# Optimization experiments

Hardware: AMD Instinct MI355X
Metric: run time of the kernel (lower is better)

Reference implementation:

```python
import jax, jax.numpy as jnp
import numpy as np

H = 256  # hidden size

def _lstm_layer(x, W_ih, W_hh, b_ih, b_hh):
    """x: [B, T, I] -> outputs [B, T, H]. PyTorch gate order: i, f, g, o."""
    B, T, _ = x.shape
    # Precompute input projections for all timesteps at once: [B, T, 4H]
    xg = jnp.einsum('bti,gi->btg', x, W_ih) + (b_ih + b_hh)
    xg = jnp.transpose(xg, (1, 0, 2))  # [T, B, 4H]

    def step(carry, xg_t):
        h, c = carry
        gates = xg_t + h @ W_hh.T  # [B, 4H]
        i = jax.nn.sigmoid(gates[:, 0 * H:1 * H])
        f = jax.nn.sigmoid(gates[:, 1 * H:2 * H])
        g = jnp.tanh(gates[:, 2 * H:3 * H])
        o = jax.nn.sigmoid(gates[:, 3 * H:4 * H])
        c = f * c + i * g
        h = o * jnp.tanh(c)
        return (h, c), h

    h0 = jnp.zeros((B, H), dtype=x.dtype)
    c0 = jnp.zeros((B, H), dtype=x.dtype)
    _, ys = jax.lax.scan(step, (h0, c0), xg)  # ys: [T, B, H]
    return jnp.transpose(ys, (1, 0, 2))


def setup_inputs() -> dict:
    key = jax.random.key(0)
    ks = jax.random.split(key, 9)
    B, T, I = 256, 512, 32
    s_in = 1.0 / np.sqrt(H)
    return {
        'M': jax.random.normal(ks[0], (B, T, I), dtype=jnp.float32),
        'W_ih0': jax.random.normal(ks[1], (4 * H, I), dtype=jnp.float32) * s_in,
        'W_hh0': jax.random.normal(ks[2], (4 * H, H), dtype=jnp.float32) * s_in,
        'b_ih0': jax.random.normal(ks[3], (4 * H,), dtype=jnp.float32) * s_in,
        'b_hh0': jax.random.normal(ks[4], (4 * H,), dtype=jnp.float32) * s_in,
        'W_ih1': jax.random.normal(ks[5], (4 * H, H), dtype=jnp.float32) * s_in,
        'W_hh1': jax.random.normal(ks[6], (4 * H, H), dtype=jnp.float32) * s_in,
        'b_ih1': jax.random.normal(ks[7], (4 * H,), dtype=jnp.float32) * s_in,
        'b_hh1': jax.random.normal(ks[8], (4 * H,), dtype=jnp.float32) * s_in,
    }


def reference(M, W_ih0, W_hh0, b_ih0, b_hh0, W_ih1, W_hh1, b_ih1, b_hh1):
    # observations_preprocessor = Identity
    x = _lstm_layer(M, W_ih0, W_hh0, b_ih0, b_hh0)
    x = _lstm_layer(x, W_ih1, W_hh1, b_ih1, b_hh1)
    # hn = rnn_out[:, -1, :]
    return x[:, -1, :]
```

## Files before the change

### kernel.cpp

```cpp
#include <hip/hip_runtime.h>
#include <hip/hip_fp16.h>


#define TT 512
#define HH 256
#define GS 294912

typedef _Float16 f16x8 __attribute__((ext_vector_type(8)));
typedef float    f32x4 __attribute__((ext_vector_type(4)));
typedef unsigned u32x4 __attribute__((ext_vector_type(4)));

__device__ __forceinline__ f16x8 cvt8(const float* p) {
  const float4 a = *(const float4*)p;
  const float4 b = *(const float4*)(p + 4);
  f16x8 r;
  r[0]=(_Float16)a.x; r[1]=(_Float16)a.y; r[2]=(_Float16)a.z; r[3]=(_Float16)a.w;
  r[4]=(_Float16)b.x; r[5]=(_Float16)b.y; r[6]=(_Float16)b.z; r[7]=(_Float16)b.w;
  return r;
}
__device__ __forceinline__ float sigm(float x){ return 1.f/(1.f + __expf(-x)); }
__device__ __forceinline__ float tanh_(float x){ return 1.f - 2.f/(1.f + __expf(2.f*x)); }

__device__ __forceinline__ u32x4 ld16(const void* p) {
  u32x4 r;
  asm volatile("global_load_dwordx4 %0, %1, off sc0 sc1"
               : "=v"(r) : "v"(p) : "memory");
  return r;
}
__device__ __forceinline__ void st2(void* p, unsigned v) {
  asm volatile("global_store_short %0, %1, off sc0 sc1"
               :: "v"(p), "v"(v) : "memory");
}
__device__ __forceinline__ void stp(void* p, unsigned v) {
  asm volatile("global_store_dword %0, %1, off sc0 sc1"
               :: "v"(p), "v"(v) : "memory");
}
__device__ __forceinline__ unsigned ldp(const void* p) {
  unsigned r;
  asm volatile("global_load_dword %0, %1, off sc0 sc1\n\ts_waitcnt vmcnt(0)"
               : "=v"(r) : "v"(p) : "memory");
  return r;
}
__device__ __forceinline__ u32x4 ldp4(const void* p) {
  u32x4 r;
  asm volatile("global_load_dwordx4 %0, %1, off sc0 sc1\n\ts_waitcnt vmcnt(0)"
               : "=v"(r) : "v"(p) : "memory");
  return r;
}
__device__ __forceinline__ void wvm0() {
  asm volatile("s_waitcnt vmcnt(0)" ::: "memory");
  __builtin_amdgcn_sched_barrier(0);
}
__device__ __forceinline__ void barrier_lds() {
  __builtin_amdgcn_sched_barrier(0);
  asm volatile("s_waitcnt lgkmcnt(0)" ::: "memory");
  __builtin_amdgcn_s_barrier();
  __builtin_amdgcn_sched_barrier(0);
}

__global__ void init_ws(uint4* p, int n) {
  int i = blockIdx.x * blockDim.x + threadIdx.x;
  if (i >= n) return;
  int rem = i % (GS / 16);
  p[i] = (rem < 17408) ? make_uint4(0x00010001u,0x00010001u,0x00010001u,0x00010001u)
                       : make_uint4(0u,0u,0u,0u);
}

__global__ __launch_bounds__(256, 1) void lstm_v16(
    const float* __restrict__ M,
    const float* __restrict__ Wih0, const float* __restrict__ Whh0,
    const float* __restrict__ bih0, const float* __restrict__ bhh0,
    const float* __restrict__ Wih1, const float* __restrict__ Whh1,
    const float* __restrict__ bih1, const float* __restrict__ bhh1,
    float* __restrict__ out, char* __restrict__ ws)
{
  __shared__ __align__(16) char ldsA[16384];
  __shared__ __align__(16) char ldsB[16384];

  const int tid  = threadIdx.x, lane = tid & 63, wv = tid >> 6;
  const int bid  = blockIdx.x;
  const int g    = bid / 12;
  const int idx  = bid - g * 12;
  const int role = idx >> 2;
  const int q4   = idx & 3;
  const int col16 = lane & 15, ko8 = (lane >> 4) << 3, brow = (lane >> 4) << 2;
  const int unit = q4 * 64 + wv * 16 + col16;

  char* base   = ws + (size_t)g * GS;
  char* stream = base;
  char* h1r    = base + 131072;
  char* xg     = base + 147456;
  int*  prog   = (int*)(base + 278528);

  const unsigned ubase = ((unsigned)(unit >> 5) << 10)
                       | ((unsigned)((unit >> 3) & 3) << 8)
                       | ((unsigned)(unit & 7) << 1);

  f16x8 W[4][8], WI[4];
  float bias[4] = {0.f, 0.f, 0.f, 0.f};
  {
    const float* Wsrc = (role == 0) ? Whh0 : (role == 1) ? Wih1 : Whh1;
    #pragma unroll
    for (int q = 0; q < 4; ++q) {
      const int row = q * HH + unit;
      #pragma unroll
      for (int kt = 0; kt < 8; ++kt)
        W[q][kt] = cvt8(Wsrc + (size_t)row * HH + kt * 32 + ko8);
      if (role == 0) { WI[q] = cvt8(Wih0 + (size_t)row * 32 + ko8);
                       bias[q] = bih0[row] + bhh0[row]; }
      else if (role == 1) bias[q] = bih1[row] + bhh1[row];
    }
  }

  float cst[4] = {0.f, 0.f, 0.f, 0.f};

  if (role == 0) {
    const float* mp = M + (size_t)(g * 16 + col16) * TT * 32 + ko8;
    float4 m0 = *(const float4*)mp, m1 = *(const float4*)(mp + 4);
    int lastW = 0;
    for (int t = 0; t < TT; ++t) {
      const int par = t & 1;
      if (t >= 1) {
        const char* s = stream + (size_t)((t - 1) & 15) * 8192 + tid * 16;
        const unsigned pat = (((unsigned)(t - 1) >> 4) & 1u) * 0x00010001u;
        u32x4 v0 = ld16(s), v1 = ld16(s + 4096);
        wvm0();
        for (;;) {
          const u32x4 d = ((v0 ^ pat) | (v1 ^ pat)) & 0x00010001u;
          if (__all((d[0] | d[1] | d[2] | d[3]) == 0)) break;
          v0 = ld16(s); v1 = ld16(s + 4096);
          wvm0();
        }
        *(u32x4*)(ldsA + par * 8192 + tid * 16)        = v0;
        *(u32x4*)(ldsA + par * 8192 + tid * 16 + 4096) = v1;
      }
      barrier_lds();
      f32x4 acc[4];
      f16x8 am;
      am[0]=(_Float16)m0.x; am[1]=(_Float16)m0.y; am[2]=(_Float16)m0.z; am[3]=(_Float16)m0.w;
      am[4]=(_Float16)m1.x; am[5]=(_Float16)m1.y; am[6]=(_Float16)m1.z; am[7]=(_Float16)m1.w;
      #pragma unroll
      for (int q = 0; q < 4; ++q) {
        acc[q] = (f32x4){bias[q], bias[q], bias[q], bias[q]};
        acc[q] = __builtin_amdgcn_mfma_f32_16x16x32_f16(am, WI[q], acc[q], 0, 0, 0);
      }
      if (t >= 1) {
        #pragma unroll
        for (int kt = 0; kt < 8; ++kt) {
          const f16x8 A = *(const f16x8*)(ldsA + par * 8192 + kt * 1024 + lane * 16);
          #pragma unroll
          for (int q = 0; q < 4; ++q)
            acc[q] = __builtin_amdgcn_mfma_f32_16x16x32_f16(A, W[q][kt], acc[q], 0, 0, 0);
        }
      }
      if (t + 1 < TT) { m0 = *(const float4*)(mp + (t + 1) * 32);
                        m1 = *(const float4*)(mp + (t + 1) * 32 + 4); }
      if (t >= 16) {
        while (lastW < t - 15) {
          const u32x4 d = ldp4(prog);
          int m = (int)d[0];
          m = m < (int)d[1] ? m : (int)d[1];
          m = m < (int)d[2] ? m : (int)d[2];
          m = m < (int)d[3] ? m : (int)d[3];
          lastW = m;
        }
      }
      char* slot = stream + (size_t)(t & 15) * 8192;
      const unsigned wt = ((unsigned)t >> 4) & 1u;
      #pragma unroll
      for (int r = 0; r < 4; ++r) {
        const float iv = sigm(acc[0][r]), fv = sigm(acc[1][r]);
        const float gv = tanh_(acc[2][r]), ov = sigm(acc[3][r]);
        cst[r] = fv * cst[r] + iv * gv;
        const float h = ov * tanh_(cst[r]);
        unsigned short hb = __builtin_bit_cast(unsigned short, (_Float16)h);
        hb = (unsigned short)((hb & 0xFFFEu) | wt);
        st2(slot + ubase + ((unsigned)(brow + r) << 4), (unsigned)hb);
      }
    }
  } else if (role == 1) {
    int lastL = 0;
    for (int t = 0; t < TT; ++t) {
      const int par = t & 1;
      {
        const char* s = stream + (size_t)(t & 15) * 8192 + tid * 16;
        const unsigned pat = (((unsigned)t >> 4) & 1u) * 0x00010001u;
        u32x4 v0 = ld16(s), v1 = ld16(s + 4096);
        wvm0();
        for (;;) {
          const u32x4 d = ((v0 ^ pat) | (v1 ^ pat)) & 0x00010001u;
          if (__all((d[0] | d[1] | d[2] | d[3]) == 0)) break;
          v0 = ld16(s); v1 = ld16(s + 4096);
          wvm0();
        }
        *(u32x4*)(ldsA + par * 8192 + tid * 16)        = v0;
        *(u32x4*)(ldsA + par * 8192 + tid * 16 + 4096) = v1;
      }
      barrier_lds();
      if (tid == 0) stp(prog + q4, (unsigned)(t + 1));
      if (t >= 4) { while (lastL < t - 3) lastL = (int)ldp(prog + 4 + q4); }
      f32x4 acc[4];
      #pragma unroll
      for (int q = 0; q < 4; ++q)
        acc[q] = (f32x4){bias[q], bias[q], bias[q], bias[q]};
      #pragma unroll
      for (int kt = 0; kt < 8; ++kt) {
        const f16x8 A = *(const f16x8*)(ldsA + par * 8192 + kt * 1024 + lane * 16);
        #pragma unroll
        for (int q = 0; q < 4; ++q)
          acc[q] = __builtin_amdgcn_mfma_f32_16x16x32_f16(A, W[q][kt], acc[q], 0, 0, 0);
      }
      char* xs = xg + (size_t)(t & 3) * 32768 + q4 * 8192;
      const unsigned wtx = ((unsigned)t >> 2) & 1u;
      #pragma unroll
      for (int q = 0; q < 4; ++q)
        #pragma unroll
        for (int r = 0; r < 4; ++r) {
          unsigned short hb = __builtin_bit_cast(unsigned short, (_Float16)acc[q][r]);
          hb = (unsigned short)((hb & 0xFFFEu) | wtx);
          const unsigned off = (unsigned)(brow + r) * 512
                             + (unsigned)(q * 64 + wv * 16 + col16) * 2;
          st2(xs + off, (unsigned)hb);
        }
    }
  } else {
    for (int t = 0; t < TT; ++t) {
      const int par = t & 1;
      {
        const char* sx = xg + (size_t)(t & 3) * 32768 + q4 * 8192 + tid * 16;
        const unsigned patX = (((unsigned)t >> 2) & 1u) * 0x00010001u;
        const char* sh = h1r + (size_t)((t - 1) & 1) * 8192 + tid * 16;
        const unsigned patH = (((unsigned)(t - 1) >> 1) & 1u) * 0x00010001u;
        const bool hasH = (t >= 1);
        u32x4 x0 = ld16(sx), x1 = ld16(sx + 4096), h0v, h1v;
        if (hasH) { h0v = ld16(sh); h1v = ld16(sh + 4096); }
        wvm0();
        for (;;) {
          u32x4 d = ((x0 ^ patX) | (x1 ^ patX)) & 0x00010001u;
          unsigned bad = d[0] | d[1] | d[2] | d[3];
          if (hasH) {
            const u32x4 e = ((h0v ^ patH) | (h1v ^ patH)) & 0x00010001u;
            bad |= e[0] | e[1] | e[2] | e[3];
          }
          if (__all(bad == 0)) break;
          x0 = ld16(sx); x1 = ld16(sx + 4096);
          if (hasH) { h0v = ld16(sh); h1v = ld16(sh + 4096); }
          wvm0();
        }
        *(u32x4*)(ldsB + par * 8192 + tid * 16)        = x0;
        *(u32x4*)(ldsB + par * 8192 + tid * 16 + 4096) = x1;
        if (hasH) {
          *(u32x4*)(ldsA + par * 8192 + tid * 16)        = h0v;
          *(u32x4*)(ldsA + par * 8192 + tid * 16 + 4096) = h1v;
        }
      }
      barrier_lds();
      if (tid == 0) stp(prog + 4 + q4, (unsigned)(t + 1));
      f32x4 acc[4];
      #pragma unroll
      for (int q = 0; q < 4; ++q) acc[q] = (f32x4){0.f, 0.f, 0.f, 0.f};
      if (t >= 1) {
        #pragma unroll
        for (int kt = 0; kt < 8; ++kt) {
          const f16x8 A = *(const f16x8*)(ldsA + par * 8192 + kt * 1024 + lane * 16);
          #pragma unroll
          for (int q = 0; q < 4; ++q)
            acc[q] = __builtin_amdgcn_mfma_f32_16x16x32_f16(A, W[q][kt], acc[q], 0, 0, 0);
        }
      }
      const char* xl = ldsB + par * 8192;
      #pragma unroll
      for (int q = 0; q < 4; ++q)
        #pragma unroll
        for (int r = 0; r < 4; ++r) {
          const unsigned short xv = *(const unsigned short*)
            (xl + (brow + r) * 512 + (q * 64 + wv * 16 + col16) * 2);
          acc[q][r] += (float)__builtin_bit_cast(_Float16, xv);
        }
      char* d1 = h1r + (size_t)par * 8192;
      const unsigned wt = ((unsigned)t >> 1) & 1u;
      #pragma unroll
      for (int r = 0; r < 4; ++r) {
        const float iv = sigm(acc[0][r]), fv = sigm(acc[1][r]);
        const float gv = tanh_(acc[2][r]), ov = sigm(acc[3][r]);
        cst[r] = fv * cst[r] + iv * gv;
        const float h = ov * tanh_(cst[r]);
        if (t < TT - 1) {
          unsigned short hb = __builtin_bit_cast(unsigned short, (_Float16)h);
          hb = (unsigned short)((hb & 0xFFFEu) | wt);
          st2(d1 + ubase + ((unsigned)(brow + r) << 4), (unsigned)hb);
        } else {
          out[(size_t)(g * 16 + brow + r) * HH + unit] = h;
        }
      }
    }
  }
}

__global__ void fb_init(uint4* p, int n) {
  int i = blockIdx.x * blockDim.x + threadIdx.x;
  if (i < n) p[i] = make_uint4(0x00010001u,0x00010001u,0x00010001u,0x00010001u);
}
__device__ __forceinline__ unsigned fb_tg(int t){ return ((unsigned)(t + 4) >> 1) & 1u; }

__global__ __launch_bounds__(512) void lstm_v9(
    const float* __restrict__ M,
    const float* __restrict__ Wih0, const float* __restrict__ Whh0,
    const float* __restrict__ bih0, const float* __restrict__ bhh0,
    const float* __restrict__ Wih1, const float* __restrict__ Whh1,
    const float* __restrict__ bih1, const float* __restrict__ bhh1,
    float* __restrict__ out, char* __restrict__ ws)
{
  __shared__ __align__(16) char  ldsA[16384];
  __shared__ __align__(16) f32x4 xch[8][64];
  const int tid  = threadIdx.x, lane = tid & 63, wv = tid >> 6;
  const int g = blockIdx.x & 7, w = blockIdx.x >> 3;
  const int hf = wv & 1, role = wv >> 1;
  const int col16 = lane & 15, ko8 = (lane >> 4) << 3;
  const int unit = w * 16 + col16;
  #define H0R(slot) (ws + (((g << 1) | (slot)) << 14))
  #define H1R(slot) (ws + 262144 + (((g << 1) | (slot)) << 14))
  f16x8 W0[4][8], WI[4];
  float bias[4] = {0.f, 0.f, 0.f, 0.f};
  if (role == 0) {
    #pragma unroll
    for (int q = 0; q < 4; ++q) {
      const int row = q * HH + unit;
      #pragma unroll
      for (int kt = 0; kt < 8; ++kt) W0[q][kt] = cvt8(Whh0 + (size_t)row*HH + kt*32 + ko8);
      WI[q] = cvt8(Wih0 + (size_t)row*32 + ko8); bias[q] = bih0[row] + bhh0[row];
    }
  } else if (role == 1) {
    #pragma unroll
    for (int q = 0; q < 4; ++q) {
      const int row = q * HH + unit;
      #pragma unroll
      for (int kt = 0; kt < 8; ++kt) W0[q][kt] = cvt8(Wih1 + (size_t)row*HH + kt*32 + ko8);
      bias[q] = bih1[row] + bhh1[row];
    }
  } else if (role == 2) {
    #pragma unroll
    for (int q = 0; q < 4; ++q) {
      const int row = q * HH + unit;
      #pragma unroll
      for (int kt = 0; kt < 8; ++kt) W0[q][kt] = cvt8(Whh1 + (size_t)row*HH + kt*32 + ko8);
    }
  }
  const int sl = tid & 63, skt = (tid >> 6) & 7;
  const unsigned moff0 = (unsigned)((sl & 15) * 512 + skt * 64 + (sl >> 4) * 16);
  const unsigned moff1 = moff0 + 16 * 512;
  const unsigned lo    = (unsigned)(skt * 1024 + sl * 16);
  const unsigned hoff = (((unsigned)(hf*16 + col16)) << 9) | ((unsigned)(lane >> 4) << 4);
  unsigned soff[4];
  #pragma unroll
  for (int r = 0; r < 4; ++r)
    soff[r] = (((unsigned)(hf*16 + ((lane>>4)<<2) + r)) << 9) | ((unsigned)unit << 1);
  const float* mp = M + (size_t)(g*32 + hf*16 + col16) * TT * 32 + ko8;
  float4 m0 = {0,0,0,0}, m1 = {0,0,0,0};
  if (role == 0) { m0 = *(const float4*)mp; m1 = *(const float4*)(mp + 4); }
  float cst[4] = {0.f, 0.f, 0.f, 0.f};
  for (int p = 0; p <= TT; ++p) {
    if (p >= 1) {
      const char* s = H0R((p - 1) & 1);
      const unsigned pat = fb_tg(p - 1) * 0x00010001u;
      u32x4 v0 = ld16(s + moff0), v1 = ld16(s + moff1);
      wvm0();
      for (;;) {
        const u32x4 d = ((v0 ^ pat) | (v1 ^ pat)) & 0x00010001u;
        if (__all((d[0] | d[1] | d[2] | d[3]) == 0)) break;
        v0 = ld16(s + moff0); v1 = ld16(s + moff1); wvm0();
      }
      *(u32x4*)(ldsA + lo) = v0; *(u32x4*)(ldsA + 8192 + lo) = v1;
    }
    barrier_lds();
    f32x4 acc[4];
    if (role == 0 && p < TT) {
      f16x8 am;
      am[0]=(_Float16)m0.x; am[1]=(_Float16)m0.y; am[2]=(_Float16)m0.z; am[3]=(_Float16)m0.w;
      am[4]=(_Float16)m1.x; am[5]=(_Float16)m1.y; am[6]=(_Float16)m1.z; am[7]=(_Float16)m1.w;
      #pragma unroll
      for (int q = 0; q < 4; ++q) {
        acc[q] = (f32x4){bias[q], bias[q], bias[q], bias[q]};
        acc[q] = __builtin_amdgcn_mfma_f32_16x16x32_f16(am, WI[q], acc[q], 0, 0, 0);
      }
      if (p >= 1) {
        #pragma unroll
        for (int kt = 0; kt < 8; ++kt) {
          const f16x8 A = *(const f16x8*)(ldsA + hf*8192 + kt*1024 + lane*16);
          #pragma unroll
          for (int q = 0; q < 4; ++q)
            acc[q] = __builtin_amdgcn_mfma_f32_16x16x32_f16(A, W0[q][kt], acc[q], 0, 0, 0);
        }
      }
      char* d = H0R(p & 1);
      const unsigned wt = fb_tg(p);
      #pragma unroll
      for (int r = 0; r < 4; ++r) {
        const float iv = sigm(acc[0][r]), fv = sigm(acc[1][r]);
        const float gv = tanh_(acc[2][r]), ov = sigm(acc[3][r]);
        cst[r] = fv * cst[r] + iv * gv;
        const float h = ov * tanh_(cst[r]);
        unsigned short hb = __builtin_bit_cast(unsigned short, (_Float16)h);
        hb = (unsigned short)((hb & 0xFFFEu) | wt);
        st2(d + soff[r], (unsigned)hb);
      }
      if (p + 1 < TT) { m0 = *(const float4*)(mp + (p+1)*32); m1 = *(const float4*)(mp + (p+1)*32 + 4); }
    } else if (role == 1 && p >= 1) {
      #pragma unroll
      for (int q = 0; q < 4; ++q) acc[q] = (f32x4){bias[q], bias[q], bias[q], bias[q]};
      #pragma unroll
      for (int kt = 0; kt < 8; ++kt) {
        const f16x8 A = *(const f16x8*)(ldsA + hf*8192 + kt*1024 + lane*16);
        #pragma unroll
        for (int q = 0; q < 4; ++q)
          acc[q] = __builtin_amdgcn_mfma_f32_16x16x32_f16(A, W0[q][kt], acc[q], 0, 0, 0);
      }
    } else if (role == 2 && p >= 2) {
      const char* s = H1R(p & 1);
      const unsigned pat = fb_tg(p - 2) * 0x00010001u;
      u32x4 hb[8];
      #pragma unroll
      for (int k = 0; k < 8; ++k) hb[k] = ld16(s + hoff + k*64);
      wvm0();
      for (;;) {
        unsigned bad = 0;
        #pragma unroll
        for (int k = 0; k < 8; ++k) {
          const u32x4 d = (hb[k] ^ pat) & 0x00010001u;
          bad |= d[0] | d[1] | d[2] | d[3];
        }
        if (__all(bad == 0)) break;
        #pragma unroll
        for (int k = 0; k < 8; ++k) hb[k] = ld16(s + hoff + k*64);
        wvm0();
      }
      #pragma unroll
      for (int q = 0; q < 4; ++q) acc[q] = (f32x4){0.f, 0.f, 0.f, 0.f};
      #pragma unroll
      for (int kt = 0; kt < 8; ++kt) {
        const f16x8 A = __builtin_bit_cast(f16x8, hb[kt]);
        #pragma unroll
        for (int q = 0; q < 4; ++q)
          acc[q] = __builtin_amdgcn_mfma_f32_16x16x32_f16(A, W0[q][kt], acc[q], 0, 0, 0);
      }
      #pragma unroll
      for (int q = 0; q < 4; ++q) xch[hf*4 + q][lane] = acc[q];
    }
    barrier_lds();
    if (role == 1 && p >= 1) {
      if (p >= 2) {
        #pragma unroll
        for (int q = 0; q < 4; ++q) acc[q] = acc[q] + xch[hf*4 + q][lane];
      }
      if (p < TT) {
        char* d = H1R((p - 1) & 1);
        const unsigned wt = fb_tg(p - 1);
        #pragma unroll
        for (int r = 0; r < 4; ++r) {
          const float iv = sigm(acc[0][r]), fv = sigm(acc[1][r]);
          const float gv = tanh_(acc[2][r]), ov = sigm(acc[3][r]);
          cst[r] = fv * cst[r] + iv * gv;
          const float h = ov * tanh_(cst[r]);
          unsigned short hb = __builtin_bit_cast(unsigned short, (_Float16)h);
          hb = (unsigned short)((hb & 0xFFFEu) | wt);
          st2(d + soff[r], (unsigned)hb);
        }
      } else {
        #pragma unroll
        for (int r = 0; r < 4; ++r) {
          const float iv = sigm(acc[0][r]), fv = sigm(acc[1][r]);
          const float gv = tanh_(acc[2][r]), ov = sigm(acc[3][r]);
          cst[r] = fv * cst[r] + iv * gv;
          const float h = ov * tanh_(cst[r]);
          const int b = hf*16 + ((lane>>4)<<2) + r;
          out[(size_t)(g*32 + b) * HH + (w*16 + col16)] = h;
        }
      }
    }
  }
  #undef H0R
  #undef H1R
}

extern "C" void kernel_launch(void* const* d_in, const int* in_sizes, int n_in,
                              void* d_out, int out_size, void* d_ws, size_t ws_size,
                              hipStream_t stream) {
  (void)in_sizes; (void)n_in; (void)out_size;
  const float* M    = (const float*)d_in[0];
  const float* Wih0 = (const float*)d_in[1];
  const float* Whh0 = (const float*)d_in[2];
  const float* bih0 = (const float*)d_in[3];
  const float* bhh0 = (const float*)d_in[4];
  const float* Wih1 = (const float*)d_in[5];
  const float* Whh1 = (const float*)d_in[6];
  const float* bih1 = (const float*)d_in[7];
  const float* bhh1 = (const float*)d_in[8];

  if (ws_size >= (size_t)16 * GS) {
    const int n16 = 16 * (GS / 16);
    init_ws<<<(n16 + 255) / 256, 256, 0, stream>>>((uint4*)d_ws, n16);
    lstm_v16<<<192, 256, 0, stream>>>(M, Wih0, Whh0, bih0, bhh0,
                                      Wih1, Whh1, bih1, bhh1,
                                      (float*)d_out, (char*)d_ws);
  } else {
    if (ws_size < 524288) return;
    fb_init<<<128, 256, 0, stream>>>((uint4*)d_ws, 32768);
    lstm_v9<<<128, 512, 0, stream>>>(M, Wih0, Whh0, bih0, bhh0,
                                     Wih1, Whh1, bih1, bhh1,
                                     (float*)d_out, (char*)d_ws);
  }
}
```

Before: 1.199 ms.

## Fuse layer-1 input projection into layer-0 blocks, dropping a role

The separate role that computed the layer-1 input projection (W_ih1·h0) is merged into the layer-0 blocks. Each layer-0 block now holds both W_hh0 and W_ih1 in registers and projects h0 of the previous step right after its own recurrence step. The grid shrinks from 12 to 8 blocks per batch group, and the layer-0 back-pressure polling on the projection role's progress counters goes away. The next stream load is also issued early, before the barrier. In exchange, register pressure doubles in the layer-0 role and the projection work now sits on the layer-0 critical path.

```diff
diff --git a/kernel.cpp b/kernel.cpp
--- a/kernel.cpp
+++ b/kernel.cpp
@@ -41,12 +41,6 @@
                : "=v"(r) : "v"(p) : "memory");
   return r;
 }
-__device__ __forceinline__ u32x4 ldp4(const void* p) {
-  u32x4 r;
-  asm volatile("global_load_dwordx4 %0, %1, off sc0 sc1\n\ts_waitcnt vmcnt(0)"
-               : "=v"(r) : "v"(p) : "memory");
-  return r;
-}
 __device__ __forceinline__ void wvm0() {
   asm volatile("s_waitcnt vmcnt(0)" ::: "memory");
   __builtin_amdgcn_sched_barrier(0);
@@ -66,7 +60,7 @@
                        : make_uint4(0u,0u,0u,0u);
 }
 
-__global__ __launch_bounds__(256, 1) void lstm_v16(
+__global__ __launch_bounds__(256, 1) void lstm_v17(
     const float* __restrict__ M,
     const float* __restrict__ Wih0, const float* __restrict__ Whh0,
     const float* __restrict__ bih0, const float* __restrict__ bhh0,
@@ -79,8 +73,8 @@
 
   const int tid  = threadIdx.x, lane = tid & 63, wv = tid >> 6;
   const int bid  = blockIdx.x;
-  const int g    = bid / 12;
-  const int idx  = bid - g * 12;
+  const int g    = bid >> 3;
+  const int idx  = bid & 7;
   const int role = idx >> 2;
   const int q4   = idx & 3;
   const int col16 = lane & 15, ko8 = (lane >> 4) << 3, brow = (lane >> 4) << 2;
@@ -96,19 +90,28 @@
                        | ((unsigned)((unit >> 3) & 3) << 8)
                        | ((unsigned)(unit & 7) << 1);
 
-  f16x8 W[4][8], WI[4];
-  float bias[4] = {0.f, 0.f, 0.f, 0.f};
-  {
-    const float* Wsrc = (role == 0) ? Whh0 : (role == 1) ? Wih1 : Whh1;
+  f16x8 W0[4][8], W1q[4][8], WI[4];
+  float bias0[4] = {0,0,0,0}, bias1[4] = {0,0,0,0};
+  if (role == 0) {
     #pragma unroll
     for (int q = 0; q < 4; ++q) {
       const int row = q * HH + unit;
       #pragma unroll
+      for (int kt = 0; kt < 8; ++kt) {
+        W0[q][kt]  = cvt8(Whh0 + (size_t)row * HH + kt * 32 + ko8);
+        W1q[q][kt] = cvt8(Wih1 + (size_t)row * HH + kt * 32 + ko8);
+      }
+      WI[q]    = cvt8(Wih0 + (size_t)row * 32 + ko8);
+      bias0[q] = bih0[row] + bhh0[row];
+      bias1[q] = bih1[row] + bhh1[row];
+    }
+  } else {
+    #pragma unroll
+    for (int q = 0; q < 4; ++q) {
+      const int row = q * HH + unit;
+      #pragma unroll
       for (int kt = 0; kt < 8; ++kt)
-        W[q][kt] = cvt8(Wsrc + (size_t)row * HH + kt * 32 + ko8);
-      if (role == 0) { WI[q] = cvt8(Wih0 + (size_t)row * 32 + ko8);
-                       bias[q] = bih0[row] + bhh0[row]; }
-      else if (role == 1) bias[q] = bih1[row] + bhh1[row];
+        W0[q][kt] = cvt8(Whh1 + (size_t)row * HH + kt * 32 + ko8);
     }
   }
 
@@ -117,13 +120,13 @@
   if (role == 0) {
     const float* mp = M + (size_t)(g * 16 + col16) * TT * 32 + ko8;
     float4 m0 = *(const float4*)mp, m1 = *(const float4*)(mp + 4);
-    int lastW = 0;
-    for (int t = 0; t < TT; ++t) {
-      const int par = t & 1;
+    int lastL = 0;
+    u32x4 v0, v1;
+    for (int t = 0; t <= TT; ++t) {
+      const int par = (t - 1) & 1;
       if (t >= 1) {
         const char* s = stream + (size_t)((t - 1) & 15) * 8192 + tid * 16;
         const unsigned pat = (((unsigned)(t - 1) >> 4) & 1u) * 0x00010001u;
-        u32x4 v0 = ld16(s), v1 = ld16(s + 4096);
         wvm0();
         for (;;) {
           const u32x4 d = ((v0 ^ pat) | (v1 ^ pat)) & 0x00010001u;
@@ -135,93 +138,70 @@
         *(u32x4*)(ldsA + par * 8192 + tid * 16 + 4096) = v1;
       }
       barrier_lds();
-      f32x4 acc[4];
-      f16x8 am;
-      am[0]=(_Float16)m0.x; am[1]=(_Float16)m0.y; am[2]=(_Float16)m0.z; am[3]=(_Float16)m0.w;
-      am[4]=(_Float16)m1.x; am[5]=(_Float16)m1.y; am[6]=(_Float16)m1.z; am[7]=(_Float16)m1.w;
-      #pragma unroll
-      for (int q = 0; q < 4; ++q) {
-        acc[q] = (f32x4){bias[q], bias[q], bias[q], bias[q]};
-        acc[q] = __builtin_amdgcn_mfma_f32_16x16x32_f16(am, WI[q], acc[q], 0, 0, 0);
+      if (t < TT) {
+        f32x4 acc[4];
+        f16x8 am;
+        am[0]=(_Float16)m0.x; am[1]=(_Float16)m0.y; am[2]=(_Float16)m0.z; am[3]=(_Float16)m0.w;
+        am[4]=(_Float16)m1.x; am[5]=(_Float16)m1.y; am[6]=(_Float16)m1.z; am[7]=(_Float16)m1.w;
+        #pragma unroll
+        for (int q = 0; q < 4; ++q) {
+          acc[q] = (f32x4){bias0[q], bias0[q], bias0[q], bias0[q]};
+          acc[q] = __builtin_amdgcn_mfma_f32_16x16x32_f16(am, WI[q], acc[q], 0, 0, 0);
+        }
+        if (t >= 1) {
+          #pragma unroll
+          for (int kt = 0; kt < 8; ++kt) {
+            const f16x8 A = *(const f16x8*)(ldsA + par * 8192 + kt * 1024 + lane * 16);
+            #pragma unroll
+            for (int q = 0; q < 4; ++q)
+              acc[q] = __builtin_amdgcn_mfma_f32_16x16x32_f16(A, W0[q][kt], acc[q], 0, 0, 0);
+          }
+        }
+        if (t + 1 < TT) { m0 = *(const float4*)(mp + (t + 1) * 32);
+                          m1 = *(const float4*)(mp + (t + 1) * 32 + 4); }
+        char* slot = stream + (size_t)(t & 15) * 8192;
+        const unsigned wt = ((unsigned)t >> 4) & 1u;
+        #pragma unroll
+        for (int r = 0; r < 4; ++r) {
+          const float iv = sigm(acc[0][r]), fv = sigm(acc[1][r]);
+          const float gv = tanh_(acc[2][r]), ov = sigm(acc[3][r]);
+          cst[r] = fv * cst[r] + iv * gv;
+          const float h = ov * tanh_(cst[r]);
+          unsigned short hb = __builtin_bit_cast(unsigned short, (_Float16)h);
+          hb = (unsigned short)((hb & 0xFFFEu) | wt);
+          st2(slot + ubase + ((unsigned)(brow + r) << 4), (unsigned)hb);
+        }
+        const char* sn = stream + (size_t)(t & 15) * 8192 + tid * 16;
+        v0 = ld16(sn); v1 = ld16(sn + 4096);
       }
       if (t >= 1) {
+        f32x4 axg[4];
+        #pragma unroll
+        for (int q = 0; q < 4; ++q)
+          axg[q] = (f32x4){bias1[q], bias1[q], bias1[q], bias1[q]};
         #pragma unroll
         for (int kt = 0; kt < 8; ++kt) {
           const f16x8 A = *(const f16x8*)(ldsA + par * 8192 + kt * 1024 + lane * 16);
           #pragma unroll
           for (int q = 0; q < 4; ++q)
-            acc[q] = __builtin_amdgcn_mfma_f32_16x16x32_f16(A, W[q][kt], acc[q], 0, 0, 0);
-        }
-      }
-      if (t + 1 < TT) { m0 = *(const float4*)(mp + (t + 1) * 32);
-                        m1 = *(const float4*)(mp + (t + 1) * 32 + 4); }
-      if (t >= 16) {
-        while (lastW < t - 15) {
-          const u32x4 d = ldp4(prog);
-          int m = (int)d[0];
-          m = m < (int)d[1] ? m : (int)d[1];
-          m = m < (int)d[2] ? m : (int)d[2];
-          m = m < (int)d[3] ? m : (int)d[3];
-          lastW = m;
-        }
-      }
-      char* slot = stream + (size_t)(t & 15) * 8192;
-      const unsigned wt = ((unsigned)t >> 4) & 1u;
-      #pragma unroll
-      for (int r = 0; r < 4; ++r) {
-        const float iv = sigm(acc[0][r]), fv = sigm(acc[1][r]);
-        const float gv = tanh_(acc[2][r]), ov = sigm(acc[3][r]);
-        cst[r] = fv * cst[r] + iv * gv;
-        const float h = ov * tanh_(cst[r]);
-        unsigned short hb = __builtin_bit_cast(unsigned short, (_Float16)h);
-        hb = (unsigned short)((hb & 0xFFFEu) | wt);
-        st2(slot + ubase + ((unsigned)(brow + r) << 4), (unsigned)hb);
-      }
-    }
-  } else if (role == 1) {
-    int lastL = 0;
-    for (int t = 0; t < TT; ++t) {
-      const int par = t & 1;
-      {
-        const char* s = stream + (size_t)(t & 15) * 8192 + tid * 16;
-        const unsigned pat = (((unsigned)t >> 4) & 1u) * 0x00010001u;
-        u32x4 v0 = ld16(s), v1 = ld16(s + 4096);
-        wvm0();
-        for (;;) {
-          const u32x4 d = ((v0 ^ pat) | (v1 ^ pat)) & 0x00010001u;
-          if (__all((d[0] | d[1] | d[2] | d[3]) == 0)) break;
-          v0 = ld16(s); v1 = ld16(s + 4096);
-          wvm0();
-        }
-        *(u32x4*)(ldsA + par * 8192 + tid * 16)        = v0;
-        *(u32x4*)(ldsA + par * 8192 + tid * 16 + 4096) = v1;
-      }
-      barrier_lds();
-      if (tid == 0) stp(prog + q4, (unsigned)(t + 1));
-      if (t >= 4) { while (lastL < t - 3) lastL = (int)ldp(prog + 4 + q4); }
-      f32x4 acc[4];
-      #pragma unroll
-      for (int q = 0; q < 4; ++q)
-        acc[q] = (f32x4){bias[q], bias[q], bias[q], bias[q]};
-      #pragma unroll
-      for (int kt = 0; kt < 8; ++kt) {
-        const f16x8 A = *(const f16x8*)(ldsA + par * 8192 + kt * 1024 + lane * 16);
+            axg[q] = __builtin_amdgcn_mfma_f32_16x16x32_f16(A, W1q[q][kt], axg[q], 0, 0, 0);
+        }
+        if (t >= 5) {
+          while (lastL < t - 4) lastL = (int)ldp(prog + 4 + q4);
+        }
+        char* xs = xg + (size_t)((t - 1) & 3) * 32768 + q4 * 8192;
+        const unsigned wtx = (((unsigned)(t - 1)) >> 2) & 1u;
         #pragma unroll
         for (int q = 0; q < 4; ++q)
-          acc[q] = __builtin_amdgcn_mfma_f32_16x16x32_f16(A, W[q][kt], acc[q], 0, 0, 0);
-      }
-      char* xs = xg + (size_t)(t & 3) * 32768 + q4 * 8192;
-      const unsigned wtx = ((unsigned)t >> 2) & 1u;
-      #pragma unroll
-      for (int q = 0; q < 4; ++q)
-        #pragma unroll
-        for (int r = 0; r < 4; ++r) {
-          unsigned short hb = __builtin_bit_cast(unsigned short, (_Float16)acc[q][r]);
-          hb = (unsigned short)((hb & 0xFFFEu) | wtx);
-          const unsigned off = (unsigned)(brow + r) * 512
-                             + (unsigned)(q * 64 + wv * 16 + col16) * 2;
-          st2(xs + off, (unsigned)hb);
-        }
+          #pragma unroll
+          for (int r = 0; r < 4; ++r) {
+            unsigned short hb = __builtin_bit_cast(unsigned short, (_Float16)axg[q][r]);
+            hb = (unsigned short)((hb & 0xFFFEu) | wtx);
+            const unsigned off = (unsigned)(brow + r) * 512
+                               + (unsigned)(q * 64 + wv * 16 + col16) * 2;
+            st2(xs + off, (unsigned)hb);
+          }
+      }
     }
   } else {
     for (int t = 0; t < TT; ++t) {
@@ -265,7 +245,7 @@
           const f16x8 A = *(const f16x8*)(ldsA + par * 8192 + kt * 1024 + lane * 16);
           #pragma unroll
           for (int q = 0; q < 4; ++q)
-            acc[q] = __builtin_amdgcn_mfma_f32_16x16x32_f16(A, W[q][kt], acc[q], 0, 0, 0);
+            acc[q] = __builtin_amdgcn_mfma_f32_16x16x32_f16(A, W0[q][kt], acc[q], 0, 0, 0);
         }
       }
       const char* xl = ldsB + par * 8192;
@@ -499,7 +479,7 @@
   if (ws_size >= (size_t)16 * GS) {
     const int n16 = 16 * (GS / 16);
     init_ws<<<(n16 + 255) / 256, 256, 0, stream>>>((uint4*)d_ws, n16);
-    lstm_v16<<<192, 256, 0, stream>>>(M, Wih0, Whh0, bih0, bhh0,
+    lstm_v17<<<128, 256, 0, stream>>>(M, Wih0, Whh0, bih0, bhh0,
                                       Wih1, Whh1, bih1, bhh1,
                                       (float*)d_out, (char*)d_ws);
   } else {
```

Result: slower. 1.570 ms (+31.0%).
